# Kernel optimization log

Measured on AMD Instinct MI355X. Metric: run time of the kernel, lower is better.

The kernel has to match this reference:

```python
import jax, jax.numpy as jnp
import numpy as np

OUT_FEATURES = 64
KERNEL_DIMS = 16


def setup_inputs() -> dict:
    key = jax.random.key(0)
    k1, k2, k3, k4 = jax.random.split(key, 4)
    N, L, F = 256, 64, 32            # in_features = L*F = 2048
    OK = OUT_FEATURES * KERNEL_DIMS  # 1024
    x = jax.random.normal(k1, (N, L, F), dtype=jnp.float32)
    W = jax.random.normal(k2, (OK, L * F), dtype=jnp.float32) * 0.02
    b = jax.random.normal(k3, (OK,), dtype=jnp.float32) * 0.02
    u = jax.random.normal(k4, (OK,), dtype=jnp.float32)
    return {"x": x, "W": W, "b": b, "u": u}


def _l2normalize(a, eps=1e-12):
    return a / (jnp.linalg.norm(a) + eps)


def reference(x, W, b, u):
    N, L, F = x.shape
    xf = x.reshape(N, L * F)
    # spectral norm: one power iteration (u, v detached, as in torch)
    W_ng = jax.lax.stop_gradient(W)
    v = _l2normalize(W_ng.T @ u)
    u_new = _l2normalize(W_ng @ v)
    sigma = u_new @ (W @ v)          # differentiable in W
    W_sn = W / sigma
    # projection: (N, out, k)
    m = (xf @ W_sn.T + b).reshape(N, OUT_FEATURES, KERNEL_DIMS)
    # all-pairs L1 distance over kernel dim -> (N, N, out)
    norm = jnp.abs(m[:, None, :, :] - m[None, :, :, :]).sum(-1)
    o_b = jnp.exp(-norm).sum(0) - 1.0          # (N, out); self term exp(0)=1 removed
    o_b = jnp.broadcast_to(o_b[:, None, :], (N, L, OUT_FEATURES))
    return jnp.concatenate([x, o_b], axis=-1)  # (N, L, F + out)
```

## Files before the change

### kernel.cpp

```cpp
#include <hip/hip_runtime.h>
#include <hip/hip_bf16.h>
#include <math.h>

#define KIN  2048
#define OKD  1024
#define NB   256
#define OUTF 64
#define KD   16

typedef float f32x4  __attribute__((ext_vector_type(4)));
typedef short bf16x4 __attribute__((ext_vector_type(4)));
typedef short bf16x8 __attribute__((ext_vector_type(8)));
typedef unsigned short u16x8 __attribute__((ext_vector_type(8)));

static __device__ __forceinline__ unsigned short f2bf(float f) {
    union { __hip_bfloat16 b; unsigned short u; } cv;
    cv.b = __float2bfloat16(f);
    return cv.u;
}
static __device__ __forceinline__ u16x8 pack8(float4 a, float4 b) {
    u16x8 r;
    r[0]=f2bf(a.x); r[1]=f2bf(a.y); r[2]=f2bf(a.z); r[3]=f2bf(a.w);
    r[4]=f2bf(b.x); r[5]=f2bf(b.y); r[6]=f2bf(b.z); r[7]=f2bf(b.w);
    return r;
}
static __device__ __forceinline__ float bf2f(unsigned short u) {
    union { unsigned int i; float f; } cv; cv.i = ((unsigned int)u) << 16; return cv.f;
}

__global__ __launch_bounds__(256) void k_vraw_cast(const float* __restrict__ W,
        const float* __restrict__ u, float* __restrict__ partial,
        unsigned short* __restrict__ Wb) {
    int tid = threadIdx.x;
    int row0 = blockIdx.x * 8;
    int c = tid * 8;
    float s[8];
#pragma unroll
    for (int i = 0; i < 8; ++i) s[i] = 0.f;
#pragma unroll
    for (int r = 0; r < 8; ++r) {
        int row = row0 + r;
        const float4* src = (const float4*)(W + (size_t)row * KIN + c);
        float4 f0 = src[0], f1 = src[1];
        *(u16x8*)(Wb + (size_t)row * KIN + c) = pack8(f0, f1);
        float uu = u[row];
        s[0] += f0.x * uu; s[1] += f0.y * uu; s[2] += f0.z * uu; s[3] += f0.w * uu;
        s[4] += f1.x * uu; s[5] += f1.y * uu; s[6] += f1.z * uu; s[7] += f1.w * uu;
    }
    float4* dst = (float4*)(partial + (size_t)blockIdx.x * KIN + c);
    dst[0] = make_float4(s[0], s[1], s[2], s[3]);
    dst[1] = make_float4(s[4], s[5], s[6], s[7]);
}

__global__ __launch_bounds__(256) void k_vredx(const float* __restrict__ partial,
        float* __restrict__ partial2, const float* __restrict__ x,
        unsigned short* __restrict__ xb) {
    int bid = blockIdx.x, tid = threadIdx.x;
    if (bid >= 16) {
        int g = (bid - 16) * 256 + tid;
        const float4* s = (const float4*)x + (size_t)g * 2;
        float4 f0 = s[0], f1 = s[1];
        *((u16x8*)xb + g) = pack8(f0, f1);
        return;
    }
    int cg = bid & 7, bg = bid >> 3;
    int col = cg * 256 + tid;
    float a = 0.f;
#pragma unroll 8
    for (int i = 0; i < 64; ++i)
        a += partial[(size_t)(bg * 64 + i) * KIN + col];
    partial2[bg * KIN + col] = a;
}

__global__ void k_vnorm(const float* __restrict__ partial2, float* __restrict__ v) {
    __shared__ float wsum[4];
    int tid = threadIdx.x;
    float a[8];
    float ss = 0.f;
#pragma unroll
    for (int q = 0; q < 8; ++q) {
        int col = tid + q * 256;
        a[q] = partial2[col] + partial2[KIN + col];
        ss += a[q] * a[q];
    }
#pragma unroll
    for (int off = 32; off; off >>= 1) ss += __shfl_xor(ss, off);
    if ((tid & 63) == 0) wsum[tid >> 6] = ss;
    __syncthreads();
    float tot = wsum[0] + wsum[1] + wsum[2] + wsum[3];
    float inv = 1.f / (sqrtf(tot) + 1e-12f);
#pragma unroll
    for (int q = 0; q < 8; ++q) v[tid + q * 256] = a[q] * inv;
}

__global__ __launch_bounds__(256) void k_t(const unsigned short* __restrict__ Wb,
        const float* __restrict__ v, float* __restrict__ tpart) {
    __shared__ float part[4];
    int tid = threadIdx.x, lane = tid & 63, w = tid >> 6;
    int row = blockIdx.x * 2 + (w >> 1);
    int h = w & 1;
    const u16x8* W8 = (const u16x8*)(Wb + (size_t)row * KIN + h * 1024);
    const float4* v4 = (const float4*)(v + h * 1024);
    float s = 0.f;
#pragma unroll
    for (int q = 0; q < 2; ++q) {
        u16x8 a = W8[q * 64 + lane];
        float4 b0 = v4[(q * 64 + lane) * 2];
        float4 b1 = v4[(q * 64 + lane) * 2 + 1];
        s += bf2f(a[0]) * b0.x + bf2f(a[1]) * b0.y + bf2f(a[2]) * b0.z + bf2f(a[3]) * b0.w;
        s += bf2f(a[4]) * b1.x + bf2f(a[5]) * b1.y + bf2f(a[6]) * b1.z + bf2f(a[7]) * b1.w;
    }
#pragma unroll
    for (int off = 32; off; off >>= 1) s += __shfl_xor(s, off);
    if (lane == 0) part[w] = s;
    __syncthreads();
    if (tid == 0) {
        float r0 = part[0] + part[1], r1 = part[2] + part[3];
        tpart[blockIdx.x] = r0 * r0 + r1 * r1;
    }
}

static __device__ __forceinline__ bf16x8 load_frag(const unsigned short* lds, int row, int k0) {
    int b0 = (row << 7) + (k0 << 1);
    b0 ^= (row & 7) << 4;
    bf16x4 lo = *(const bf16x4*)((const char*)lds + b0);
    bf16x4 hi = *(const bf16x4*)((const char*)lds + (b0 ^ 32));
    bf16x8 r;
    r[0]=lo[0]; r[1]=lo[1]; r[2]=lo[2]; r[3]=lo[3];
    r[4]=hi[0]; r[5]=hi[1]; r[6]=hi[2]; r[7]=hi[3];
    return r;
}

__global__ __launch_bounds__(256) void k_gemm(const unsigned short* __restrict__ xb,
        const unsigned short* __restrict__ Wb, const float* __restrict__ tpart,
        const float* __restrict__ bias, float* __restrict__ M) {
    __shared__ unsigned short sAB[4096];
    __shared__ float red[4];
    __shared__ float s_inv;
    int tid = threadIdx.x;
    int lane = tid & 63, w = tid >> 6;
    int c0 = blockIdx.x * 32, n0 = blockIdx.y * 32;

    float sv = tpart[tid] + tpart[tid + 256];
#pragma unroll
    for (int off = 32; off; off >>= 1) sv += __shfl_xor(sv, off);
    if (lane == 0) red[w] = sv;
    __syncthreads();
    if (tid == 0) {
        float ssq = red[0] + red[1] + red[2] + red[3];
        s_inv = (sqrtf(ssq) + 1e-12f) / ssq;
    }

    const char* gq[2];
    unsigned short* lq[2];
#pragma unroll
    for (int q = 0; q < 2; ++q) {
        int ch = q * 4 + w;
        int p = ch * 1024 + lane * 16;
        int rp = p & 4095;
        int row = rp >> 7;
        int off = (rp & 127) ^ ((row & 7) << 4);
        const unsigned short* base = (p < 4096) ? xb : Wb;
        int grow = (p < 4096) ? (n0 + row) : (c0 + row);
        gq[q] = (const char*)(base + (size_t)grow * KIN) + off;
        lq[q] = sAB + ch * 512;
    }

    int g = lane >> 4, cl = lane & 15;
    int wy = w >> 1, wx = w & 1;
    f32x4 acc;
#pragma unroll
    for (int r = 0; r < 4; ++r) acc[r] = 0.f;

    const unsigned short* sA = sAB;
    const unsigned short* sB = sAB + 2048;

    for (int t = 0; t < 32; ++t) {
        int kbyte = t * 128;
        __syncthreads();
#pragma unroll
        for (int q = 0; q < 2; ++q)
            __builtin_amdgcn_global_load_lds(
                (const __attribute__((address_space(1))) unsigned int*)(gq[q] + kbyte),
                (__attribute__((address_space(3))) unsigned int*)lq[q], 16, 0, 0);
        __syncthreads();
#pragma unroll
        for (int s = 0; s < 2; ++s) {
            int k0 = s * 32 + 4 * g;
            bf16x8 af = load_frag(sA, wy * 16 + cl, k0);
            bf16x8 bf = load_frag(sB, wx * 16 + cl, k0);
            acc = __builtin_amdgcn_mfma_f32_16x16x32_bf16(af, bf, acc, 0, 0, 0);
        }
    }

    float inv = s_inv;
    int col = c0 + wx * 16 + cl;
    float bb = bias[col];
    int row0 = n0 + wy * 16 + 4 * g;
#pragma unroll
    for (int r = 0; r < 4; ++r)
        M[(size_t)(row0 + r) * OKD + col] = acc[r] * inv + bb;
}

__global__ __launch_bounds__(256) void k_pair(const float* __restrict__ M,
                                              float* __restrict__ ob) {
    __shared__ float sm[NB * KD];
    int o = blockIdx.x, tid = threadIdx.x;
    const float4* M4 = (const float4*)M;
    float4* sm4 = (float4*)sm;
#pragma unroll
    for (int tq = 0; tq < 4; ++tq) {
        int idx = tid + tq * 256;
        int j = idx >> 2, k4 = idx & 3;
        sm4[j * 4 + (k4 ^ (j & 3))] = M4[(size_t)j * 256 + o * 4 + k4];
    }
    __syncthreads();
    int n = blockIdx.y * 32 + (tid >> 3);
    int jc = tid & 7;
    int nx = (n & 3) << 2;
    float r[KD];
#pragma unroll
    for (int k = 0; k < KD; ++k) r[k] = sm[n * 16 + (k ^ nx)];
    float acc = 0.f;
    for (int jj = 0; jj < 32; ++jj) {
        int j = jj * 8 + jc;
        int base = j * 16, jx = (j & 3) << 2;
        float d = 0.f;
#pragma unroll
        for (int k = 0; k < KD; ++k) d += fabsf(r[k] - sm[base + (k ^ jx)]);
        acc += __expf(-d);
    }
    acc += __shfl_xor(acc, 1);
    acc += __shfl_xor(acc, 2);
    acc += __shfl_xor(acc, 4);
    if (jc == 0) ob[n * OUTF + o] = acc - 1.0f;
}

__global__ void k_out(const float* __restrict__ X, const float* __restrict__ ob,
                      float4* __restrict__ out4) {
    int q = blockIdx.x * 256 + threadIdx.x;
    int r = q / 24;
    int c = q - r * 24;
    if (c < 8) {
        out4[q] = ((const float4*)X)[(size_t)r * 8 + c];
    } else {
        int n = r >> 6;
        out4[q] = ((const float4*)ob)[n * 16 + (c - 8)];
    }
}

extern "C" void kernel_launch(void* const* d_in, const int* in_sizes, int n_in,
                              void* d_out, int out_size, void* d_ws, size_t ws_size,
                              hipStream_t stream) {
    const float* x = (const float*)d_in[0];
    const float* W = (const float*)d_in[1];
    const float* b = (const float*)d_in[2];
    const float* u = (const float*)d_in[3];

    float* ws = (float*)d_ws;
    float* M        = ws;
    float* partial  = ws;
    float* ob       = ws + 262144;
    float* partial2 = ws + 262144;
    float* v        = ws + 278528;
    float* tpart    = ws + 280576;
    unsigned short* Wb = (unsigned short*)(ws + 281088);
    unsigned short* xb = (unsigned short*)(ws + 1329664);

    k_vraw_cast<<<128, 256, 0, stream>>>(W, u, partial, Wb);
    k_vredx    <<<272, 256, 0, stream>>>(partial, partial2, x, xb);
    k_vnorm    <<<1,   256, 0, stream>>>(partial2, v);
    k_t        <<<512, 256, 0, stream>>>(Wb, v, tpart);
    k_gemm     <<<dim3(32, 8), 256, 0, stream>>>(xb, Wb, tpart, b, M);
    k_pair     <<<dim3(64, 8), 256, 0, stream>>>(M, ob);
    k_out      <<<1536, 256, 0, stream>>>(x, ob, (float4*)d_out);
}
```

Measured before the change: 104.8 us.

## Fuse spectral-norm stages, double-buffer GEMM, fold scale and bias into pair kernel

Merges the W cast and u-weighted partial sums with the x cast and the x copy into the output into one stage kernel. It also fuses the W·v row-norm work into the GEMM launch. Normalizing v is skipped: the unnormalized norm is computed and divided out later. The GEMM now double-buffers its LDS tiles so the next k-slice loads while the current one computes. The 1/sigma scale is applied inside the exp of the pair kernel, and the bias is dropped because it cancels in pairwise differences. This cuts the launch count and the serial dependency chain, at the cost of more index logic and some divergent block roles.

```diff
diff --git a/kernel.cpp b/kernel.cpp
--- a/kernel.cpp
+++ b/kernel.cpp
@@ -28,96 +28,61 @@
     union { unsigned int i; float f; } cv; cv.i = ((unsigned int)u) << 16; return cv.f;
 }
 
-__global__ __launch_bounds__(256) void k_vraw_cast(const float* __restrict__ W,
-        const float* __restrict__ u, float* __restrict__ partial,
-        unsigned short* __restrict__ Wb) {
-    int tid = threadIdx.x;
-    int row0 = blockIdx.x * 8;
-    int c = tid * 8;
-    float s[8];
-#pragma unroll
-    for (int i = 0; i < 8; ++i) s[i] = 0.f;
-#pragma unroll
-    for (int r = 0; r < 8; ++r) {
-        int row = row0 + r;
-        const float4* src = (const float4*)(W + (size_t)row * KIN + c);
-        float4 f0 = src[0], f1 = src[1];
-        *(u16x8*)(Wb + (size_t)row * KIN + c) = pack8(f0, f1);
-        float uu = u[row];
-        s[0] += f0.x * uu; s[1] += f0.y * uu; s[2] += f0.z * uu; s[3] += f0.w * uu;
-        s[4] += f1.x * uu; s[5] += f1.y * uu; s[6] += f1.z * uu; s[7] += f1.w * uu;
-    }
-    float4* dst = (float4*)(partial + (size_t)blockIdx.x * KIN + c);
-    dst[0] = make_float4(s[0], s[1], s[2], s[3]);
-    dst[1] = make_float4(s[4], s[5], s[6], s[7]);
-}
-
-__global__ __launch_bounds__(256) void k_vredx(const float* __restrict__ partial,
-        float* __restrict__ partial2, const float* __restrict__ x,
-        unsigned short* __restrict__ xb) {
-    int bid = blockIdx.x, tid = threadIdx.x;
-    if (bid >= 16) {
-        int g = (bid - 16) * 256 + tid;
-        const float4* s = (const float4*)x + (size_t)g * 2;
-        float4 f0 = s[0], f1 = s[1];
-        *((u16x8*)xb + g) = pack8(f0, f1);
-        return;
-    }
-    int cg = bid & 7, bg = bid >> 3;
+__global__ __launch_bounds__(256) void k_stage1(const float* __restrict__ W,
+        const float* __restrict__ u, const float* __restrict__ x,
+        float* __restrict__ partial, unsigned short* __restrict__ Wb,
+        unsigned short* __restrict__ xb, float4* __restrict__ out4) {
+    int bid = blockIdx.x, tid = threadIdx.x;
+    if (bid < 256) {
+        int row0 = bid * 4;
+        int c = tid * 8;
+        float s[8];
+#pragma unroll
+        for (int i = 0; i < 8; ++i) s[i] = 0.f;
+#pragma unroll
+        for (int r = 0; r < 4; ++r) {
+            int row = row0 + r;
+            const float4* src = (const float4*)(W + (size_t)row * KIN + c);
+            float4 f0 = src[0], f1 = src[1];
+            *(u16x8*)(Wb + (size_t)row * KIN + c) = pack8(f0, f1);
+            float uu = u[row];
+            s[0] += f0.x * uu; s[1] += f0.y * uu; s[2] += f0.z * uu; s[3] += f0.w * uu;
+            s[4] += f1.x * uu; s[5] += f1.y * uu; s[6] += f1.z * uu; s[7] += f1.w * uu;
+        }
+        float4* dst = (float4*)(partial + (size_t)bid * KIN + c);
+        dst[0] = make_float4(s[0], s[1], s[2], s[3]);
+        dst[1] = make_float4(s[4], s[5], s[6], s[7]);
+    } else if (bid < 288) {
+        int xc = bid - 256;
+        const float4* x4 = (const float4*)x;
+#pragma unroll
+        for (int p = 0; p < 8; ++p) {
+            int g = xc * 2048 + p * 256 + tid;
+            float4 f0 = x4[(size_t)g * 2], f1 = x4[(size_t)g * 2 + 1];
+            *((u16x8*)xb + g) = pack8(f0, f1);
+        }
+    } else {
+        int xo = bid - 288;
+        const float4* x4 = (const float4*)x;
+#pragma unroll
+        for (int p = 0; p < 4; ++p) {
+            int i = xo * 1024 + p * 256 + tid;
+            int r = i >> 3, c = i & 7;
+            out4[(size_t)r * 24 + c] = x4[i];
+        }
+    }
+}
+
+__global__ __launch_bounds__(256) void k_vred(const float* __restrict__ partial,
+                                              float* __restrict__ partial2) {
+    int bid = blockIdx.x, tid = threadIdx.x;
+    int bg = bid & 1, cg = bid >> 1;
     int col = cg * 256 + tid;
     float a = 0.f;
 #pragma unroll 8
-    for (int i = 0; i < 64; ++i)
-        a += partial[(size_t)(bg * 64 + i) * KIN + col];
+    for (int i = 0; i < 128; ++i)
+        a += partial[(size_t)(bg * 128 + i) * KIN + col];
     partial2[bg * KIN + col] = a;
-}
-
-__global__ void k_vnorm(const float* __restrict__ partial2, float* __restrict__ v) {
-    __shared__ float wsum[4];
-    int tid = threadIdx.x;
-    float a[8];
-    float ss = 0.f;
-#pragma unroll
-    for (int q = 0; q < 8; ++q) {
-        int col = tid + q * 256;
-        a[q] = partial2[col] + partial2[KIN + col];
-        ss += a[q] * a[q];
-    }
-#pragma unroll
-    for (int off = 32; off; off >>= 1) ss += __shfl_xor(ss, off);
-    if ((tid & 63) == 0) wsum[tid >> 6] = ss;
-    __syncthreads();
-    float tot = wsum[0] + wsum[1] + wsum[2] + wsum[3];
-    float inv = 1.f / (sqrtf(tot) + 1e-12f);
-#pragma unroll
-    for (int q = 0; q < 8; ++q) v[tid + q * 256] = a[q] * inv;
-}
-
-__global__ __launch_bounds__(256) void k_t(const unsigned short* __restrict__ Wb,
-        const float* __restrict__ v, float* __restrict__ tpart) {
-    __shared__ float part[4];
-    int tid = threadIdx.x, lane = tid & 63, w = tid >> 6;
-    int row = blockIdx.x * 2 + (w >> 1);
-    int h = w & 1;
-    const u16x8* W8 = (const u16x8*)(Wb + (size_t)row * KIN + h * 1024);
-    const float4* v4 = (const float4*)(v + h * 1024);
-    float s = 0.f;
-#pragma unroll
-    for (int q = 0; q < 2; ++q) {
-        u16x8 a = W8[q * 64 + lane];
-        float4 b0 = v4[(q * 64 + lane) * 2];
-        float4 b1 = v4[(q * 64 + lane) * 2 + 1];
-        s += bf2f(a[0]) * b0.x + bf2f(a[1]) * b0.y + bf2f(a[2]) * b0.z + bf2f(a[3]) * b0.w;
-        s += bf2f(a[4]) * b1.x + bf2f(a[5]) * b1.y + bf2f(a[6]) * b1.z + bf2f(a[7]) * b1.w;
-    }
-#pragma unroll
-    for (int off = 32; off; off >>= 1) s += __shfl_xor(s, off);
-    if (lane == 0) part[w] = s;
-    __syncthreads();
-    if (tid == 0) {
-        float r0 = part[0] + part[1], r1 = part[2] + part[3];
-        tpart[blockIdx.x] = r0 * r0 + r1 * r1;
-    }
 }
 
 static __device__ __forceinline__ bf16x8 load_frag(const unsigned short* lds, int row, int k0) {
@@ -131,28 +96,50 @@
     return r;
 }
 
-__global__ __launch_bounds__(256) void k_gemm(const unsigned short* __restrict__ xb,
-        const unsigned short* __restrict__ Wb, const float* __restrict__ tpart,
-        const float* __restrict__ bias, float* __restrict__ M) {
-    __shared__ unsigned short sAB[4096];
-    __shared__ float red[4];
-    __shared__ float s_inv;
-    int tid = threadIdx.x;
+__global__ __launch_bounds__(256) void k_tg(const unsigned short* __restrict__ xb,
+        const unsigned short* __restrict__ Wb, const float* __restrict__ partial2,
+        float* __restrict__ tpart, float* __restrict__ P) {
+    __shared__ unsigned short sAB[2][4096];
+    __shared__ float part[4], part2s[4];
+    int bid = blockIdx.x, tid = threadIdx.x;
     int lane = tid & 63, w = tid >> 6;
-    int c0 = blockIdx.x * 32, n0 = blockIdx.y * 32;
-
-    float sv = tpart[tid] + tpart[tid + 256];
-#pragma unroll
-    for (int off = 32; off; off >>= 1) sv += __shfl_xor(sv, off);
-    if (lane == 0) red[w] = sv;
-    __syncthreads();
-    if (tid == 0) {
-        float ssq = red[0] + red[1] + red[2] + red[3];
-        s_inv = (sqrtf(ssq) + 1e-12f) / ssq;
-    }
+
+    if (bid >= 256) {
+        int tb = bid - 256;
+        int row = tb * 2 + (w >> 1);
+        int h = w & 1;
+        const u16x8* W8 = (const u16x8*)(Wb + (size_t)row * KIN + h * 1024);
+        const float4* pa = (const float4*)(partial2 + h * 1024);
+        const float4* pb = (const float4*)(partial2 + KIN + h * 1024);
+        float s = 0.f, s2 = 0.f;
+#pragma unroll
+        for (int q = 0; q < 2; ++q) {
+            int idx = q * 64 + lane;
+            u16x8 a = W8[idx];
+            float4 a0 = pa[idx * 2], a1 = pa[idx * 2 + 1];
+            float4 b0 = pb[idx * 2], b1 = pb[idx * 2 + 1];
+            float v0 = a0.x + b0.x, v1 = a0.y + b0.y, v2 = a0.z + b0.z, v3 = a0.w + b0.w;
+            float v4 = a1.x + b1.x, v5 = a1.y + b1.y, v6 = a1.z + b1.z, v7 = a1.w + b1.w;
+            s += bf2f(a[0])*v0 + bf2f(a[1])*v1 + bf2f(a[2])*v2 + bf2f(a[3])*v3;
+            s += bf2f(a[4])*v4 + bf2f(a[5])*v5 + bf2f(a[6])*v6 + bf2f(a[7])*v7;
+            s2 += v0*v0 + v1*v1 + v2*v2 + v3*v3 + v4*v4 + v5*v5 + v6*v6 + v7*v7;
+        }
+#pragma unroll
+        for (int off = 32; off; off >>= 1) { s += __shfl_xor(s, off); s2 += __shfl_xor(s2, off); }
+        if (lane == 0) { part[w] = s; part2s[w] = s2; }
+        __syncthreads();
+        if (tid == 0) {
+            float r0 = part[0] + part[1], r1 = part[2] + part[3];
+            tpart[tb] = r0 * r0 + r1 * r1;
+            if (tb == 0) tpart[512] = part2s[0] + part2s[1];
+        }
+        return;
+    }
+
+    int c0 = (bid & 31) * 32, n0 = (bid >> 5) * 32;
 
     const char* gq[2];
-    unsigned short* lq[2];
+    int lqo[2];
 #pragma unroll
     for (int q = 0; q < 2; ++q) {
         int ch = q * 4 + w;
@@ -163,7 +150,7 @@
         const unsigned short* base = (p < 4096) ? xb : Wb;
         int grow = (p < 4096) ? (n0 + row) : (c0 + row);
         gq[q] = (const char*)(base + (size_t)grow * KIN) + off;
-        lq[q] = sAB + ch * 512;
+        lqo[q] = ch * 512;
     }
 
     int g = lane >> 4, cl = lane & 15;
@@ -172,18 +159,25 @@
 #pragma unroll
     for (int r = 0; r < 4; ++r) acc[r] = 0.f;
 
-    const unsigned short* sA = sAB;
-    const unsigned short* sB = sAB + 2048;
+#pragma unroll
+    for (int q = 0; q < 2; ++q)
+        __builtin_amdgcn_global_load_lds(
+            (const __attribute__((address_space(1))) unsigned int*)(gq[q]),
+            (__attribute__((address_space(3))) unsigned int*)(&sAB[0][lqo[q]]), 16, 0, 0);
+    __syncthreads();
 
     for (int t = 0; t < 32; ++t) {
-        int kbyte = t * 128;
-        __syncthreads();
-#pragma unroll
-        for (int q = 0; q < 2; ++q)
-            __builtin_amdgcn_global_load_lds(
-                (const __attribute__((address_space(1))) unsigned int*)(gq[q] + kbyte),
-                (__attribute__((address_space(3))) unsigned int*)lq[q], 16, 0, 0);
-        __syncthreads();
+        int cur = t & 1;
+        if (t < 31) {
+            int kb = (t + 1) * 128;
+#pragma unroll
+            for (int q = 0; q < 2; ++q)
+                __builtin_amdgcn_global_load_lds(
+                    (const __attribute__((address_space(1))) unsigned int*)(gq[q] + kb),
+                    (__attribute__((address_space(3))) unsigned int*)(&sAB[cur ^ 1][lqo[q]]), 16, 0, 0);
+        }
+        const unsigned short* sA = sAB[cur];
+        const unsigned short* sB = sAB[cur] + 2048;
 #pragma unroll
         for (int s = 0; s < 2; ++s) {
             int k0 = s * 32 + 4 * g;
@@ -191,21 +185,27 @@
             bf16x8 bf = load_frag(sB, wx * 16 + cl, k0);
             acc = __builtin_amdgcn_mfma_f32_16x16x32_bf16(af, bf, acc, 0, 0, 0);
         }
-    }
-
-    float inv = s_inv;
+        __syncthreads();
+    }
+
     int col = c0 + wx * 16 + cl;
-    float bb = bias[col];
     int row0 = n0 + wy * 16 + 4 * g;
 #pragma unroll
     for (int r = 0; r < 4; ++r)
-        M[(size_t)(row0 + r) * OKD + col] = acc[r] * inv + bb;
+        P[(size_t)(row0 + r) * OKD + col] = acc[r];
 }
 
 __global__ __launch_bounds__(256) void k_pair(const float* __restrict__ M,
-                                              float* __restrict__ ob) {
+        const float* __restrict__ tpart, float* __restrict__ ob) {
     __shared__ float sm[NB * KD];
+    __shared__ float sred[4];
     int o = blockIdx.x, tid = threadIdx.x;
+
+    float tv = tpart[tid] + tpart[tid + 256];
+#pragma unroll
+    for (int off = 32; off; off >>= 1) tv += __shfl_xor(tv, off);
+    if ((tid & 63) == 0) sred[tid >> 6] = tv;
+
     const float4* M4 = (const float4*)M;
     float4* sm4 = (float4*)sm;
 #pragma unroll
@@ -215,6 +215,12 @@
         sm4[j * 4 + (k4 ^ (j & 3))] = M4[(size_t)j * 256 + o * 4 + k4];
     }
     __syncthreads();
+
+    float ssum = sred[0] + sred[1] + sred[2] + sred[3];
+    float nv2 = tpart[512];
+    float ssq = ssum / nv2;
+    float invs = (sqrtf(ssq) + 1e-12f) / ssq;
+
     int n = blockIdx.y * 32 + (tid >> 3);
     int jc = tid & 7;
     int nx = (n & 3) << 2;
@@ -228,7 +234,7 @@
         float d = 0.f;
 #pragma unroll
         for (int k = 0; k < KD; ++k) d += fabsf(r[k] - sm[base + (k ^ jx)]);
-        acc += __expf(-d);
+        acc += __expf(-d * invs);
     }
     acc += __shfl_xor(acc, 1);
     acc += __shfl_xor(acc, 2);
@@ -236,16 +242,14 @@
     if (jc == 0) ob[n * OUTF + o] = acc - 1.0f;
 }
 
-__global__ void k_out(const float* __restrict__ X, const float* __restrict__ ob,
-                      float4* __restrict__ out4) {
-    int q = blockIdx.x * 256 + threadIdx.x;
-    int r = q / 24;
-    int c = q - r * 24;
-    if (c < 8) {
-        out4[q] = ((const float4*)X)[(size_t)r * 8 + c];
-    } else {
-        int n = r >> 6;
-        out4[q] = ((const float4*)ob)[n * 16 + (c - 8)];
+__global__ void k_obout(const float* __restrict__ ob, float4* __restrict__ out4) {
+    int bid = blockIdx.x, tid = threadIdx.x;
+    const float4* ob4 = (const float4*)ob;
+#pragma unroll
+    for (int p = 0; p < 4; ++p) {
+        int i = bid * 1024 + p * 256 + tid;
+        int r = i >> 4, c2 = i & 15;
+        out4[(size_t)r * 24 + 8 + c2] = ob4[(r >> 6) * 16 + c2];
     }
 }
 
@@ -254,24 +258,20 @@
                               hipStream_t stream) {
     const float* x = (const float*)d_in[0];
     const float* W = (const float*)d_in[1];
-    const float* b = (const float*)d_in[2];
     const float* u = (const float*)d_in[3];
 
     float* ws = (float*)d_ws;
-    float* M        = ws;
     float* partial  = ws;
-    float* ob       = ws + 262144;
-    float* partial2 = ws + 262144;
-    float* v        = ws + 278528;
-    float* tpart    = ws + 280576;
-    unsigned short* Wb = (unsigned short*)(ws + 281088);
-    unsigned short* xb = (unsigned short*)(ws + 1329664);
-
-    k_vraw_cast<<<128, 256, 0, stream>>>(W, u, partial, Wb);
-    k_vredx    <<<272, 256, 0, stream>>>(partial, partial2, x, xb);
-    k_vnorm    <<<1,   256, 0, stream>>>(partial2, v);
-    k_t        <<<512, 256, 0, stream>>>(Wb, v, tpart);
-    k_gemm     <<<dim3(32, 8), 256, 0, stream>>>(xb, Wb, tpart, b, M);
-    k_pair     <<<dim3(64, 8), 256, 0, stream>>>(M, ob);
-    k_out      <<<1536, 256, 0, stream>>>(x, ob, (float4*)d_out);
-}
+    float* P        = ws;
+    float* partial2 = ws + 524288;
+    float* tpart    = ws + 528384;
+    float* ob       = ws + 529408;
+    unsigned short* Wb = (unsigned short*)(ws + 545792);
+    unsigned short* xb = (unsigned short*)(ws + 1594368);
+
+    k_stage1<<<416, 256, 0, stream>>>(W, u, x, partial, Wb, xb, (float4*)d_out);
+    k_vred  <<<16,  256, 0, stream>>>(partial, partial2);
+    k_tg    <<<768, 256, 0, stream>>>(xb, Wb, partial2, tpart, P);
+    k_pair  <<<dim3(64, 8), 256, 0, stream>>>(P, tpart, ob);
+    k_obout <<<256, 256, 0, stream>>>(ob, (float4*)d_out);
+}
```

Result: faster. 102.3 us (-2.5%).
